# Optimization experiments

Measured on AMD Instinct MI355X. Metric: run time of the kernel, lower is better.

The kernel has to match this reference:

```python
import jax, jax.numpy as jnp
import numpy as np

N, C, D = 8192, 6, 512


def setup_inputs() -> dict:
    key = jax.random.key(0)
    k1, k2, k3, k4 = jax.random.split(key, 4)
    logits = jax.random.normal(k1, (N, C), dtype=jnp.float32)      # unused by the loss
    targets = jax.random.uniform(k2, (N, C), dtype=jnp.float32)    # soft labels
    features = jax.random.normal(k3, (N, D), dtype=jnp.float32)
    weights = jax.random.uniform(k4, (N,), dtype=jnp.float32)
    t = jnp.asarray(10.0, dtype=jnp.float32)   # nn.Parameter init
    b = jnp.asarray(-10.0, dtype=jnp.float32)  # nn.Parameter init
    return {"logits": logits, "targets": targets, "features": features,
            "weights": weights, "t": t, "b": b}


def reference(logits, targets, features, weights, t, b):
    # F.normalize(features, p=2, dim=1) with eps=1e-12 clamp like torch
    norm = jnp.maximum(jnp.linalg.norm(features, axis=1, keepdims=True), 1e-12)
    f = features / norm                                   # [N, D]
    sim = jnp.einsum('nd,md->nm', f, f)                   # [N, N] cosine similarity
    agree = 2.0 * jnp.einsum('nc,mc->nm', targets, targets) - 1.0  # [N, N]
    elements = agree * (t * sim + b)
    # -log(1/(1+exp(e))) == softplus(e) == -log_sigmoid(-e), numerically stable
    loss = (1.0 / N) * (-jax.nn.log_sigmoid(-elements)).sum(axis=1)  # [N]
    loss = loss * weights / weights.mean()
    return loss
```

## Files before the change

### kernel.cpp

```cpp
#include <hip/hip_runtime.h>
#include <hip/hip_bf16.h>


#define NROW 8192
#define DIM  512
#define NCLS 6

#define BM 128
#define BK 64
#define NB (NROW / BM)
#define NTRI (NB * (NB + 1) / 2)
#define NSTG 8

typedef short s16x8 __attribute__((ext_vector_type(8)));
typedef float f32x4 __attribute__((ext_vector_type(4)));

static __device__ __forceinline__ ushort f2bf(float x) {
    __hip_bfloat16 h = __float2bfloat16(x);
    union { __hip_bfloat16 h; ushort u; } c; c.h = h; return c.u;
}
static __device__ __forceinline__ float bf2f(ushort u) {
    union { __hip_bfloat16 h; ushort u; } c; c.u = u; return __bfloat162float(c.h);
}

__global__ __launch_bounds__(256) void k_prep(const float* __restrict__ feat,
                                              const float* __restrict__ tgt,
                                              const float* __restrict__ w,
                                              ushort* __restrict__ fpack,
                                              ushort* __restrict__ tpA,
                                              ushort* __restrict__ tpB,
                                              float* __restrict__ partial,
                                              float* __restrict__ wpart) {
    const int wave = threadIdx.x >> 6, lane = threadIdx.x & 63;
    const int row = blockIdx.x * 4 + wave;
    const float* fr = feat + (size_t)row * DIM;
    float4 v0 = *(const float4*)(fr + lane * 4);
    float4 v1 = *(const float4*)(fr + 256 + lane * 4);
    float ss = v0.x*v0.x + v0.y*v0.y + v0.z*v0.z + v0.w*v0.w
             + v1.x*v1.x + v1.y*v1.y + v1.z*v1.z + v1.w*v1.w;
#pragma unroll
    for (int m = 1; m < 64; m <<= 1) ss += __shfl_xor(ss, m);
    const float inv = 1.f / fmaxf(sqrtf(ss), 1e-12f);

    float vals[8] = {v0.x, v0.y, v0.z, v0.w, v1.x, v1.y, v1.z, v1.w};
    ushort hi[8];
#pragma unroll
    for (int i = 0; i < 8; ++i) hi[i] = f2bf(vals[i] * inv);
    ushort* dst = fpack + (size_t)row * 512;
    *(ushort4*)(dst + lane * 4)       = make_ushort4(hi[0], hi[1], hi[2], hi[3]);
    *(ushort4*)(dst + 256 + lane * 4) = make_ushort4(hi[4], hi[5], hi[6], hi[7]);

    if (lane < 32) {
        float ta = 0.f, tb = 0.f;
        if (lane < 18) {
            int c = (lane < 6) ? lane : (lane < 12 ? lane - 6 : lane - 12);
            float x = tgt[(size_t)row * NCLS + c];
            ushort h = f2bf(x);
            float hf = bf2f(h);
            float l = x - hf;
            if (lane < 6)       { ta = hf; tb = hf; }
            else if (lane < 12) { ta = l;  tb = hf; }
            else                { ta = hf; tb = l;  }
        }
        tpA[(size_t)row * 32 + lane] = f2bf(ta);
        tpB[(size_t)row * 32 + lane] = f2bf(tb);
    }

    __shared__ float red[4];
    if (lane == 0) {
        partial[row] = 0.f;
        red[wave] = w[row];
    }
    __syncthreads();
    if (threadIdx.x == 0)
        wpart[blockIdx.x] = red[0] + red[1] + red[2] + red[3];
}

__device__ __forceinline__ void stage_f(const ushort* __restrict__ src,
                                        ushort* lds, int tid) {
#pragma unroll
    for (int i = 0; i < 4; ++i) {
        int q = i * 256 + tid;
        int r = q >> 3, c = q & 7;
        __builtin_amdgcn_global_load_lds(
            (const __attribute__((address_space(1))) void*)(src + (size_t)r * 512 + c * 8),
            (__attribute__((address_space(3))) void*)(lds + q * 8),
            16, 0, 0);
    }
}
__device__ __forceinline__ void stage_t(const ushort* __restrict__ src,
                                        ushort* lds, int tid) {
#pragma unroll
    for (int i = 0; i < 2; ++i) {
        int q = i * 256 + tid;
        int r = q >> 2, c = q & 3;
        __builtin_amdgcn_global_load_lds(
            (const __attribute__((address_space(1))) void*)(src + (size_t)r * 32 + c * 8),
            (__attribute__((address_space(3))) void*)(lds + q * 8),
            16, 0, 0);
    }
}

__global__ __launch_bounds__(256, 3) void k_gemm(
    const ushort* __restrict__ fpack, const ushort* __restrict__ tpA,
    const ushort* __restrict__ tpB, const float* __restrict__ tp,
    const float* __restrict__ bp, float* __restrict__ partial) {

    const int orig = blockIdx.x;
    int b = (orig & 7) * (NTRI / 8) + (orig >> 3);
    int SI = 0, rem = b;
    while (rem >= 36 + (7 - SI) * 64) { rem -= 36 + (7 - SI) * 64; ++SI; }
    int bi, bj;
    if (rem < 36) {
        int ii = 0;
        while (rem >= 8 - ii) { rem -= 8 - ii; ++ii; }
        bi = SI * 8 + ii;
        bj = SI * 8 + ii + rem;
    } else {
        const int r2 = rem - 36;
        const int SJ = SI + 1 + (r2 >> 6);
        const int idx = r2 & 63;
        bi = SI * 8 + (idx >> 3);
        bj = SJ * 8 + (idx & 7);
    }

    __shared__ ushort sA[BM * BK];
    __shared__ ushort sB[BM * BK];

    const int tid = threadIdx.x;
    const int lane = tid & 63;
    const int wave = tid >> 6;
    const int wr = wave >> 1, wc = wave & 1;

    const float tt = *tp, bb = *bp;

    f32x4 accS[4][4], accT[4][4];
#pragma unroll
    for (int i = 0; i < 4; ++i)
#pragma unroll
        for (int j = 0; j < 4; ++j) {
            accS[i][j] = (f32x4){0.f, 0.f, 0.f, 0.f};
            accT[i][j] = (f32x4){0.f, 0.f, 0.f, 0.f};
        }

    const ushort* baseA = fpack + (size_t)(bi * BM) * 512;
    const ushort* baseB = fpack + (size_t)(bj * BM) * 512;

    for (int s = 0; s < NSTG; ++s) {
        stage_f(baseA + s * 64, &sA[0], tid);
        stage_f(baseB + s * 64, &sB[0], tid);
        __syncthreads();
#pragma unroll
        for (int kk = 0; kk < 2; ++kk) {
            s16x8 af[4], bg[4];
            const int kb = kk * 32 + (lane >> 4) * 8;
            const int rr = lane & 15;
#pragma unroll
            for (int i = 0; i < 4; ++i)
                af[i] = *(const s16x8*)(&sA[(wr * 64 + i * 16 + rr) * BK + kb]);
#pragma unroll
            for (int j = 0; j < 4; ++j)
                bg[j] = *(const s16x8*)(&sB[(wc * 64 + j * 16 + rr) * BK + kb]);
#pragma unroll
            for (int i = 0; i < 4; ++i)
#pragma unroll
                for (int j = 0; j < 4; ++j)
                    accS[i][j] = __builtin_amdgcn_mfma_f32_16x16x32_bf16(
                        af[i], bg[j], accS[i][j], 0, 0, 0);
        }
        __syncthreads();
    }

    stage_t(tpA + (size_t)(bi * BM) * 32, &sA[0], tid);
    stage_t(tpB + (size_t)(bj * BM) * 32, &sB[0], tid);
    __syncthreads();
    {
        s16x8 af[4], bg[4];
        const int kb = (lane >> 4) * 8;
        const int rr = lane & 15;
#pragma unroll
        for (int i = 0; i < 4; ++i)
            af[i] = *(const s16x8*)(&sA[(wr * 64 + i * 16 + rr) * 32 + kb]);
#pragma unroll
        for (int j = 0; j < 4; ++j)
            bg[j] = *(const s16x8*)(&sB[(wc * 64 + j * 16 + rr) * 32 + kb]);
#pragma unroll
        for (int i = 0; i < 4; ++i)
#pragma unroll
            for (int j = 0; j < 4; ++j)
                accT[i][j] = __builtin_amdgcn_mfma_f32_16x16x32_bf16(
                    af[i], bg[j], accT[i][j], 0, 0, 0);
    }

    float rowsum[4][4];
    float colsum[4];
#pragma unroll
    for (int i = 0; i < 4; ++i)
#pragma unroll
        for (int r = 0; r < 4; ++r) rowsum[i][r] = 0.f;
#pragma unroll
    for (int j = 0; j < 4; ++j) colsum[j] = 0.f;

#pragma unroll
    for (int i = 0; i < 4; ++i)
#pragma unroll
        for (int j = 0; j < 4; ++j)
#pragma unroll
            for (int r = 0; r < 4; ++r) {
                const float agree = fmaf(2.f, accT[i][j][r], -1.f);
                const float e = agree * fmaf(tt, accS[i][j][r], bb);
                const float sp = fmaxf(e, 0.f) + __logf(1.f + __expf(-fabsf(e)));
                rowsum[i][r] += sp;
                colsum[j] += sp;
            }

#pragma unroll
    for (int i = 0; i < 4; ++i)
#pragma unroll
        for (int r = 0; r < 4; ++r) {
            float v = rowsum[i][r];
            v += __shfl_xor(v, 1); v += __shfl_xor(v, 2);
            v += __shfl_xor(v, 4); v += __shfl_xor(v, 8);
            if ((lane & 15) == 0)
                atomicAdd(&partial[bi * BM + wr * 64 + i * 16 + (lane >> 4) * 4 + r], v);
        }
    if (bi != bj) {
#pragma unroll
        for (int j = 0; j < 4; ++j) {
            float v = colsum[j];
            v += __shfl_xor(v, 16); v += __shfl_xor(v, 32);
            if (lane < 16)
                atomicAdd(&partial[bj * BM + wc * 64 + j * 16 + lane], v);
        }
    }
}

__global__ __launch_bounds__(256) void k_final(const float* __restrict__ partial,
                                               const float* __restrict__ w,
                                               const float* __restrict__ wpart,
                                               float* __restrict__ out) {
    __shared__ float red[4];
    float s = 0.f;
    for (int i = threadIdx.x; i < NROW / 4; i += 256) s += wpart[i];
#pragma unroll
    for (int m = 1; m < 64; m <<= 1) s += __shfl_xor(s, m);
    if ((threadIdx.x & 63) == 0) red[threadIdx.x >> 6] = s;
    __syncthreads();
    const float wsum = red[0] + red[1] + red[2] + red[3];
    int i = blockIdx.x * 256 + threadIdx.x;
    out[i] = partial[i] * w[i] / wsum;
}

extern "C" void kernel_launch(void* const* d_in, const int* in_sizes, int n_in,
                              void* d_out, int out_size, void* d_ws, size_t ws_size,
                              hipStream_t stream) {
    const float* targets  = (const float*)d_in[1];
    const float* features = (const float*)d_in[2];
    const float* weights  = (const float*)d_in[3];
    const float* tp       = (const float*)d_in[4];
    const float* bp       = (const float*)d_in[5];
    float* out = (float*)d_out;

    char* p = (char*)d_ws;
    ushort* fpack   = (ushort*)p; p += (size_t)NROW * 512 * sizeof(ushort);
    ushort* tpA     = (ushort*)p; p += (size_t)NROW * 32 * sizeof(ushort);
    ushort* tpB     = (ushort*)p; p += (size_t)NROW * 32 * sizeof(ushort);
    float*  partial = (float*)p;  p += (size_t)NROW * sizeof(float);
    float*  wpart   = (float*)p;  p += (size_t)(NROW / 4) * sizeof(float);

    k_prep<<<NROW / 4, 256, 0, stream>>>(features, targets, weights, fpack, tpA, tpB,
                                         partial, wpart);
    k_gemm<<<NTRI, 256, 0, stream>>>(fpack, tpA, tpB, tp, bp, partial);
    k_final<<<NROW / 256, 256, 0, stream>>>(partial, weights, wpart, out);
}
```

Before: 153.4 us.

## Double-buffer GEMM K-stages with async LDS loads and XOR-swizzled feature layout

```diff
diff --git a/kernel.cpp b/kernel.cpp
--- a/kernel.cpp
+++ b/kernel.cpp
@@ -10,7 +10,6 @@
 #define BK 64
 #define NB (NROW / BM)
 #define NTRI (NB * (NB + 1) / 2)
-#define NSTG 8
 
 typedef short s16x8 __attribute__((ext_vector_type(8)));
 typedef float f32x4 __attribute__((ext_vector_type(4)));
@@ -47,8 +46,9 @@
 #pragma unroll
     for (int i = 0; i < 8; ++i) hi[i] = f2bf(vals[i] * inv);
     ushort* dst = fpack + (size_t)row * 512;
-    *(ushort4*)(dst + lane * 4)       = make_ushort4(hi[0], hi[1], hi[2], hi[3]);
-    *(ushort4*)(dst + 256 + lane * 4) = make_ushort4(hi[4], hi[5], hi[6], hi[7]);
+    const int sw = (row & 7) << 3;
+    *(ushort4*)(dst + ((lane * 4) ^ sw))         = make_ushort4(hi[0], hi[1], hi[2], hi[3]);
+    *(ushort4*)(dst + ((256 + lane * 4) ^ sw))   = make_ushort4(hi[4], hi[5], hi[6], hi[7]);
 
     if (lane < 32) {
         float ta = 0.f, tb = 0.f;
@@ -101,7 +101,7 @@
     }
 }
 
-__global__ __launch_bounds__(256, 3) void k_gemm(
+__global__ __launch_bounds__(256, 2) void k_gemm(
     const ushort* __restrict__ fpack, const ushort* __restrict__ tpA,
     const ushort* __restrict__ tpB, const float* __restrict__ tp,
     const float* __restrict__ bp, float* __restrict__ partial) {
@@ -124,8 +124,10 @@
         bj = SJ * 8 + (idx & 7);
     }
 
-    __shared__ ushort sA[BM * BK];
-    __shared__ ushort sB[BM * BK];
+    __shared__ __align__(16) ushort sA0[BM * BK];
+    __shared__ __align__(16) ushort sB0[BM * BK];
+    __shared__ __align__(16) ushort sA1[BM * BK];
+    __shared__ __align__(16) ushort sB1[BM * BK];
 
     const int tid = threadIdx.x;
     const int lane = tid & 63;
@@ -145,45 +147,70 @@
 
     const ushort* baseA = fpack + (size_t)(bi * BM) * 512;
     const ushort* baseB = fpack + (size_t)(bj * BM) * 512;
-
-    for (int s = 0; s < NSTG; ++s) {
-        stage_f(baseA + s * 64, &sA[0], tid);
-        stage_f(baseB + s * 64, &sB[0], tid);
-        __syncthreads();
-#pragma unroll
-        for (int kk = 0; kk < 2; ++kk) {
-            s16x8 af[4], bg[4];
-            const int kb = kk * 32 + (lane >> 4) * 8;
-            const int rr = lane & 15;
-#pragma unroll
-            for (int i = 0; i < 4; ++i)
-                af[i] = *(const s16x8*)(&sA[(wr * 64 + i * 16 + rr) * BK + kb]);
-#pragma unroll
-            for (int j = 0; j < 4; ++j)
-                bg[j] = *(const s16x8*)(&sB[(wc * 64 + j * 16 + rr) * BK + kb]);
-#pragma unroll
-            for (int i = 0; i < 4; ++i)
-#pragma unroll
-                for (int j = 0; j < 4; ++j)
-                    accS[i][j] = __builtin_amdgcn_mfma_f32_16x16x32_bf16(
-                        af[i], bg[j], accS[i][j], 0, 0, 0);
-        }
-        __syncthreads();
-    }
-
-    stage_t(tpA + (size_t)(bi * BM) * 32, &sA[0], tid);
-    stage_t(tpB + (size_t)(bj * BM) * 32, &sB[0], tid);
-    __syncthreads();
+    const int rr = lane & 15;
+    const int ksw = (lane & 7) << 3;
+
+#define COMPUTE_SIM(SA, SB)                                                     \
+    do {                                                                        \
+        _Pragma("unroll")                                                       \
+        for (int kk = 0; kk < 2; ++kk) {                                        \
+            s16x8 af[4], bg[4];                                                 \
+            const int kb = (kk * 32 + ((lane >> 4) * 8)) ^ ksw;                 \
+            _Pragma("unroll")                                                   \
+            for (int i = 0; i < 4; ++i)                                         \
+                af[i] = *(const s16x8*)(&SA[(wr * 64 + i * 16 + rr) * BK + kb]);\
+            _Pragma("unroll")                                                   \
+            for (int j = 0; j < 4; ++j)                                         \
+                bg[j] = *(const s16x8*)(&SB[(wc * 64 + j * 16 + rr) * BK + kb]);\
+            _Pragma("unroll")                                                   \
+            for (int i = 0; i < 4; ++i)                                         \
+                _Pragma("unroll")                                               \
+                for (int j = 0; j < 4; ++j)                                     \
+                    accS[i][j] = __builtin_amdgcn_mfma_f32_16x16x32_bf16(       \
+                        af[i], bg[j], accS[i][j], 0, 0, 0);                     \
+        }                                                                       \
+    } while (0)
+
+#define PHASE_SYNC()                         \
+    __builtin_amdgcn_s_barrier();            \
+    __builtin_amdgcn_sched_barrier(0)
+
+    stage_f(baseA, sA0, tid);
+    stage_f(baseB, sB0, tid);
+
+#pragma unroll
+    for (int s = 0; s < 8; s += 2) {
+        stage_f(baseA + (s + 1) * 64, sA1, tid);
+        stage_f(baseB + (s + 1) * 64, sB1, tid);
+        asm volatile("s_waitcnt vmcnt(8)" ::: "memory");
+        PHASE_SYNC();
+        COMPUTE_SIM(sA0, sB0);
+        PHASE_SYNC();
+        if (s + 2 < 8) {
+            stage_f(baseA + (s + 2) * 64, sA0, tid);
+            stage_f(baseB + (s + 2) * 64, sB0, tid);
+            asm volatile("s_waitcnt vmcnt(8)" ::: "memory");
+        } else {
+            stage_t(tpA + (size_t)(bi * BM) * 32, sA0, tid);
+            stage_t(tpB + (size_t)(bj * BM) * 32, sB0, tid);
+            asm volatile("s_waitcnt vmcnt(4)" ::: "memory");
+        }
+        PHASE_SYNC();
+        COMPUTE_SIM(sA1, sB1);
+        PHASE_SYNC();
+    }
+
+    asm volatile("s_waitcnt vmcnt(0)" ::: "memory");
+    PHASE_SYNC();
     {
         s16x8 af[4], bg[4];
-        const int kb = (lane >> 4) * 8;
-        const int rr = lane & 15;
+        const int kbt = (lane >> 4) * 8;
 #pragma unroll
         for (int i = 0; i < 4; ++i)
-            af[i] = *(const s16x8*)(&sA[(wr * 64 + i * 16 + rr) * 32 + kb]);
+            af[i] = *(const s16x8*)(&sA0[(wr * 64 + i * 16 + rr) * 32 + kbt]);
 #pragma unroll
         for (int j = 0; j < 4; ++j)
-            bg[j] = *(const s16x8*)(&sB[(wc * 64 + j * 16 + rr) * 32 + kb]);
+            bg[j] = *(const s16x8*)(&sB0[(wc * 64 + j * 16 + rr) * 32 + kbt]);
 #pragma unroll
         for (int i = 0; i < 4; ++i)
 #pragma unroll
@@ -233,6 +260,8 @@
                 atomicAdd(&partial[bj * BM + wc * 64 + j * 16 + lane], v);
         }
     }
+#undef COMPUTE_SIM
+#undef PHASE_SYNC
 }
 
 __global__ __launch_bounds__(256) void k_final(const float* __restrict__ partial,
```

New measurement: 149.0 us. 1.03x faster.
